# Performance work log

Measured on AMD Instinct MI355X. Metric: run time of the kernel, lower is better.

## Reference

```python
import jax, jax.numpy as jnp
import numpy as np

H = 1024
NH = 16
HD = H // NH
TEMP = 0.5
LN_EPS = 1e-5


def setup_inputs() -> dict:
    key = jax.random.key(0)
    ks = jax.random.split(key, 11)
    s = 1.0 / np.sqrt(H)
    return {
        "feat": jax.random.normal(ks[0], (4, 2048, H), dtype=jnp.float32),
        "qw": jax.random.uniform(ks[1], (H, H), jnp.float32, -s, s),
        "qb": jax.random.uniform(ks[2], (H,), jnp.float32, -s, s),
        "kw": jax.random.uniform(ks[3], (H, H), jnp.float32, -s, s),
        "kb": jax.random.uniform(ks[4], (H,), jnp.float32, -s, s),
        "vw": jax.random.uniform(ks[5], (H, H), jnp.float32, -s, s),
        "vb": jax.random.uniform(ks[6], (H,), jnp.float32, -s, s),
        "ow": jax.random.uniform(ks[7], (H, H), jnp.float32, -s, s),
        "ob": jax.random.uniform(ks[8], (H,), jnp.float32, -s, s),
        "ln_g": jnp.ones((H,), jnp.float32),
        "ln_b": jnp.zeros((H,), jnp.float32),
    }


def reference(feat, qw, qb, kw, kb, vw, vb, ow, ob, ln_g, ln_b):
    B, S, _ = feat.shape
    # torch Linear: y = x @ W.T + b
    def split_heads(x):  # [B,S,H] -> [B,NH,S,HD]
        return x.reshape(B, S, NH, HD).transpose(0, 2, 1, 3)

    Q = split_heads(feat @ qw.T + qb)
    K = split_heads(feat @ kw.T + kb)
    V = split_heads(feat @ vw.T + vb)

    # temperature-scaled attention (note: divide by 0.5, NOT 1/sqrt(d))
    scores = jnp.einsum("bhqd,bhkd->bhqk", Q, K) / TEMP
    w = jax.nn.softmax(scores, axis=-1)
    attn = jnp.einsum("bhqk,bhkd->bhqd", w, V)  # [B,NH,S,HD]
    attn = attn.transpose(0, 2, 1, 3).reshape(B, S, H)

    out = attn @ ow.T + ob
    out = jax.nn.relu(out)  # dropout is identity in eval mode
    mu = jnp.mean(out, axis=-1, keepdims=True)
    var = jnp.mean(jnp.square(out - mu), axis=-1, keepdims=True)
    out = (out - mu) * jax.lax.rsqrt(var + LN_EPS) * ln_g + ln_b
    return out
```

## Files before the change

### kernel.cpp

```cpp
#include <hip/hip_runtime.h>
#include <math.h>

#define HDIM 1024
#define NHEAD 16
#define HEADD 64
#define SEQLEN 2048
#define BATCH 4
#define MROWS (BATCH * SEQLEN)
#define LN_EPS 1e-5f
#define QSCALE 2.8853900817779268f

typedef float f32x4 __attribute__((ext_vector_type(4)));
typedef short s16x8 __attribute__((ext_vector_type(8)));
typedef short s16x4 __attribute__((ext_vector_type(4)));
typedef __bf16 bf16x4 __attribute__((ext_vector_type(4)));

#define MFMA16(a, b, c) __builtin_amdgcn_mfma_f32_16x16x32_bf16((a), (b), (c), 0, 0, 0)

#if __has_builtin(__builtin_amdgcn_exp2f)
#define EXP2(x) __builtin_amdgcn_exp2f(x)
#else
#define EXP2(x) exp2f(x)
#endif

__device__ __forceinline__ void load_lds16(const __bf16* g, __bf16* l) {
  __builtin_amdgcn_global_load_lds((const __attribute__((address_space(1))) void*)g,
                                   (__attribute__((address_space(3))) void*)l, 16, 0, 0);
}

__global__ __launch_bounds__(256) void split_k(const float* __restrict__ src,
                                               __bf16* __restrict__ h,
                                               __bf16* __restrict__ l, int n4) {
  int i = blockIdx.x * blockDim.x + threadIdx.x;
  if (i >= n4) return;
  float4 v = reinterpret_cast<const float4*>(src)[i];
  bf16x4 hv, lv;
  hv[0] = (__bf16)v.x; hv[1] = (__bf16)v.y; hv[2] = (__bf16)v.z; hv[3] = (__bf16)v.w;
  lv[0] = (__bf16)(v.x - (float)hv[0]);
  lv[1] = (__bf16)(v.y - (float)hv[1]);
  lv[2] = (__bf16)(v.z - (float)hv[2]);
  lv[3] = (__bf16)(v.w - (float)hv[3]);
  reinterpret_cast<bf16x4*>(h)[i] = hv;
  reinterpret_cast<bf16x4*>(l)[i] = lv;
}

__global__ __launch_bounds__(256) void wsplit_k(
    const float* __restrict__ w0, const float* __restrict__ w1,
    const float* __restrict__ w2, const float* __restrict__ w3,
    __bf16* __restrict__ h0, __bf16* __restrict__ l0, __bf16* __restrict__ h1,
    __bf16* __restrict__ l1, __bf16* __restrict__ h2, __bf16* __restrict__ l2,
    __bf16* __restrict__ h3, __bf16* __restrict__ l3) {
  const int which = blockIdx.y;
  const float* src = which == 0 ? w0 : which == 1 ? w1 : which == 2 ? w2 : w3;
  __bf16* h = which == 0 ? h0 : which == 1 ? h1 : which == 2 ? h2 : h3;
  __bf16* l = which == 0 ? l0 : which == 1 ? l1 : which == 2 ? l2 : l3;
  const int i = blockIdx.x * blockDim.x + threadIdx.x;
  float4 v = reinterpret_cast<const float4*>(src)[i];
  bf16x4 hv, lv;
  hv[0] = (__bf16)v.x; hv[1] = (__bf16)v.y; hv[2] = (__bf16)v.z; hv[3] = (__bf16)v.w;
  lv[0] = (__bf16)(v.x - (float)hv[0]);
  lv[1] = (__bf16)(v.y - (float)hv[1]);
  lv[2] = (__bf16)(v.z - (float)hv[2]);
  lv[3] = (__bf16)(v.w - (float)hv[3]);
  reinterpret_cast<bf16x4*>(h)[i] = hv;
  reinterpret_cast<bf16x4*>(l)[i] = lv;
}

template <int EPI, int PASSES>
__global__ __launch_bounds__(256, 2) void gemm3p_k(
    const __bf16* __restrict__ AH, const __bf16* __restrict__ AL,
    const __bf16* __restrict__ BH, const __bf16* __restrict__ BL,
    const float* __restrict__ bias, const float scale, __bf16* __restrict__ CH,
    __bf16* __restrict__ CL, float* __restrict__ CF) {
  __shared__ __bf16 smem[(PASSES == 3) ? 32768 : 24576];

  const int tid = threadIdx.x;
  const int lane = tid & 63;
  const int w = tid >> 6;
  const int fr = lane & 15;
  const int g = lane >> 4;
  const int wm = w >> 1, wn = w & 1;
  const int m0 = blockIdx.x << 7;
  const int n0 = blockIdx.y << 7;

#define GSTAGE(buf, kt)                                                       \
  do {                                                                        \
    const int ke_ = (kt) * 32 + (lane & 3) * 8;                               \
    _Pragma("unroll") for (int c_ = 0; c_ < 2; ++c_) {                        \
      const int rr_ = 32 * w + 16 * c_ + (lane >> 2);                         \
      const int lo_ = (32 * w + 16 * c_) * 32;                                \
      load_lds16(AH + (size_t)(m0 + rr_) * HDIM + ke_, &smem[(buf)*4096 + lo_]); \
      load_lds16(AL + (size_t)(m0 + rr_) * HDIM + ke_, &smem[8192 + (buf)*4096 + lo_]); \
      load_lds16(BH + (size_t)(n0 + rr_) * HDIM + ke_, &smem[16384 + (buf)*4096 + lo_]); \
      if (PASSES == 3)                                                        \
        load_lds16(BL + (size_t)(n0 + rr_) * HDIM + ke_, &smem[24576 + (buf)*4096 + lo_]); \
    }                                                                         \
  } while (0)

  f32x4 acc[4][4] = {};

  GSTAGE(0, 0);
  __syncthreads();

  for (int kt = 0; kt < HDIM / 32; ++kt) {
    const int buf = kt & 1;
    if (kt + 1 < HDIM / 32) GSTAGE(buf ^ 1, kt + 1);

    s16x8 aH[4], aL[4], bH[4], bL[4];
#pragma unroll
    for (int mi = 0; mi < 4; ++mi) {
      const int off = (wm * 64 + mi * 16 + fr) * 32 + g * 8;
      aH[mi] = *reinterpret_cast<const s16x8*>(&smem[buf * 4096 + off]);
      aL[mi] = *reinterpret_cast<const s16x8*>(&smem[8192 + buf * 4096 + off]);
    }
#pragma unroll
    for (int ni = 0; ni < 4; ++ni) {
      const int off = (wn * 64 + ni * 16 + fr) * 32 + g * 8;
      bH[ni] = *reinterpret_cast<const s16x8*>(&smem[16384 + buf * 4096 + off]);
      if (PASSES == 3)
        bL[ni] = *reinterpret_cast<const s16x8*>(&smem[24576 + buf * 4096 + off]);
    }
#pragma unroll
    for (int mi = 0; mi < 4; ++mi)
#pragma unroll
      for (int ni = 0; ni < 4; ++ni) {
        acc[mi][ni] = MFMA16(aH[mi], bH[ni], acc[mi][ni]);
        if (PASSES == 3) acc[mi][ni] = MFMA16(aH[mi], bL[ni], acc[mi][ni]);
        acc[mi][ni] = MFMA16(aL[mi], bH[ni], acc[mi][ni]);
      }
    __syncthreads();
  }

  float bv[4];
#pragma unroll
  for (int ni = 0; ni < 4; ++ni) bv[ni] = bias[n0 + wn * 64 + ni * 16 + fr];

  if (EPI == 0) {
#pragma unroll
    for (int mi = 0; mi < 4; ++mi)
#pragma unroll
      for (int ni = 0; ni < 4; ++ni)
#pragma unroll
        for (int r = 0; r < 4; ++r) {
          const float v = (acc[mi][ni][r] + bv[ni]) * scale;
          const int m = m0 + wm * 64 + mi * 16 + 4 * g + r;
          const int n = n0 + wn * 64 + ni * 16 + fr;
          const int b = m >> 11, s = m & 2047, h = n >> 6, d = n & 63;
          const size_t o = ((size_t)(b * NHEAD + h) * SEQLEN + s) * HEADD + d;
          const __bf16 hb = (__bf16)v;
          CH[o] = hb;
          CL[o] = (__bf16)(v - (float)hb);
        }
  } else if (EPI == 2) {
#pragma unroll
    for (int mi = 0; mi < 4; ++mi)
#pragma unroll
      for (int ni = 0; ni < 4; ++ni)
#pragma unroll
        for (int r = 0; r < 4; ++r) {
          const int m = m0 + wm * 64 + mi * 16 + 4 * g + r;
          const int n = n0 + wn * 64 + ni * 16 + fr;
          CF[(size_t)m * HDIM + n] = acc[mi][ni][r] + bv[ni];
        }
  } else {
    __syncthreads();
#pragma unroll
    for (int mi = 0; mi < 4; ++mi)
#pragma unroll
      for (int ni = 0; ni < 4; ++ni)
#pragma unroll
        for (int r = 0; r < 4; ++r) {
          const float v = acc[mi][ni][r] + bv[ni];
          const int nl = wn * 64 + ni * 16 + fr;
          const int ml = wm * 64 + mi * 16 + 4 * g + r;
          smem[nl * 128 + (((ml >> 3) ^ (nl & 7)) << 3) + (ml & 7)] = (__bf16)v;
        }
    __syncthreads();
    const int nl = tid >> 1, mh = tid & 1;
    const int b = m0 >> 11, s0 = m0 & 2047;
    const int gn = n0 + nl, h = gn >> 6, d = gn & 63;
#pragma unroll
    for (int j = 0; j < 8; ++j) {
      const int cm = mh * 8 + j;
      s16x8 vv = *reinterpret_cast<const s16x8*>(&smem[nl * 128 + ((cm ^ (nl & 7)) << 3)]);
      const size_t o = ((size_t)((b * NHEAD + h) * HEADD + d)) * SEQLEN + s0 + cm * 8;
      *reinterpret_cast<s16x8*>(&CH[o]) = vv;
    }
  }
#undef GSTAGE
}

__global__ __launch_bounds__(256, 3) void attn7_k(
    const __bf16* __restrict__ QH, const __bf16* __restrict__ QL,
    const __bf16* __restrict__ KH, const __bf16* __restrict__ KL,
    const __bf16* __restrict__ VT, __bf16* __restrict__ OH,
    __bf16* __restrict__ OL) {
  __shared__ __bf16 smem[24576];

  const int tid = threadIdx.x;
  const int lane = tid & 63;
  const int w = tid >> 6;
  const int fr = lane & 15;
  const int g = lane >> 4;
  const int f7 = fr & 7;

  const int blk = blockIdx.x;
  const int xcd = blk & 7, idx = blk >> 3;
  const int bh = xcd * 8 + (idx >> 4);
  const int qt = idx & 15;
  const int q0 = qt << 7;
  const size_t bhO = (size_t)bh * SEQLEN * HEADD;

  s16x8 qHf[2][2], qLf[2][2];
#pragma unroll
  for (int qb = 0; qb < 2; ++qb) {
    const size_t qoff = bhO + (size_t)(q0 + w * 32 + qb * 16 + fr) * HEADD;
#pragma unroll
    for (int ks = 0; ks < 2; ++ks) {
      qHf[qb][ks] = *reinterpret_cast<const s16x8*>(&QH[qoff + ks * 32 + g * 8]);
      qLf[qb][ks] = *reinterpret_cast<const s16x8*>(&QL[qoff + ks * 32 + g * 8]);
    }
  }

  const __bf16* gsrc[6];
  int gstep[6], ldoff[6];
  {
    const int rsub = lane >> 3;
    const int l7 = lane & 7;
#pragma unroll
    for (int i_ = 0; i_ < 6; ++i_) {
      const int L_ = w * 6 + i_;
      const int t_ = L_ >> 3, sub_ = L_ & 7;
      ldoff[i_] = t_ * 8192 + sub_ * 512;
      if (t_ < 2) {
        const __bf16* base_ = (t_ == 0) ? KH : KL;
        const int ch_ = l7 ^ (((sub_ & 3) << 1) | (rsub & 1));
        gsrc[i_] = base_ + bhO + (size_t)(sub_ * 8 + rsub) * HEADD + ch_ * 8;
        gstep[i_] = 64 * HEADD;
      } else {
        const int ch_ = l7 ^ rsub;
        gsrc[i_] = VT + ((size_t)bh * HEADD + sub_ * 8 + rsub) * SEQLEN + ch_ * 8;
        gstep[i_] = 64;
      }
    }
  }

#define ASTAGE(bufl)                                              \
  do {                                                            \
    _Pragma("unroll") for (int i_ = 0; i_ < 6; ++i_) {            \
      load_lds16(gsrc[i_], &smem[ldoff[i_] + (bufl)*4096]);       \
      gsrc[i_] += gstep[i_];                                      \
    }                                                             \
  } while (0)

  const int sK = ((fr >> 2) << 1) | (fr & 1);
  const int rbk0 = ((fr >> 2) * 8 + (fr & 3)) * 64 + ((g ^ sK) << 3);
  const int rbk1 = rbk0 ^ 32;
  const int rbv0 = fr * 64 + ((g ^ f7) << 3);
  const int rbv1 = rbv0 ^ 32;

  f32x4 oacc0[4] = {}, oacc1[4] = {};
  float m0r = -1e30f, m1r = -1e30f, l0r = 0.f, l1r = 0.f;

  auto process = [&](const int B) {
    f32x4 sf0[4] = {}, sf1[4] = {};
    __builtin_amdgcn_s_setprio(1);
#pragma unroll
    for (int kb = 0; kb < 4; ++kb) {
      const int ko = (kb & 1) * 256 + (kb >> 1) * 2048;
      const s16x8 kh0 = *reinterpret_cast<const s16x8*>(&smem[B * 4096 + ko + rbk0]);
      const s16x8 kl0 = *reinterpret_cast<const s16x8*>(&smem[8192 + B * 4096 + ko + rbk0]);
      const s16x8 kh1 = *reinterpret_cast<const s16x8*>(&smem[B * 4096 + ko + rbk1]);
      const s16x8 kl1 = *reinterpret_cast<const s16x8*>(&smem[8192 + B * 4096 + ko + rbk1]);
      sf0[kb] = MFMA16(kh0, qHf[0][0], sf0[kb]);
      sf0[kb] = MFMA16(kl0, qHf[0][0], sf0[kb]);
      sf0[kb] = MFMA16(kh0, qLf[0][0], sf0[kb]);
      sf0[kb] = MFMA16(kh1, qHf[0][1], sf0[kb]);
      sf0[kb] = MFMA16(kl1, qHf[0][1], sf0[kb]);
      sf0[kb] = MFMA16(kh1, qLf[0][1], sf0[kb]);
      sf1[kb] = MFMA16(kh0, qHf[1][0], sf1[kb]);
      sf1[kb] = MFMA16(kl0, qHf[1][0], sf1[kb]);
      sf1[kb] = MFMA16(kh0, qLf[1][0], sf1[kb]);
      sf1[kb] = MFMA16(kh1, qHf[1][1], sf1[kb]);
      sf1[kb] = MFMA16(kl1, qHf[1][1], sf1[kb]);
      sf1[kb] = MFMA16(kh1, qLf[1][1], sf1[kb]);
    }
    __builtin_amdgcn_s_setprio(0);

    float mx0 = sf0[0][0], mx1 = sf1[0][0];
#pragma unroll
    for (int kb = 0; kb < 4; ++kb)
#pragma unroll
      for (int r = 0; r < 4; ++r) {
        mx0 = fmaxf(mx0, sf0[kb][r]);
        mx1 = fmaxf(mx1, sf1[kb][r]);
      }
    mx0 = fmaxf(mx0, __shfl_xor(mx0, 16));
    mx0 = fmaxf(mx0, __shfl_xor(mx0, 32));
    mx1 = fmaxf(mx1, __shfl_xor(mx1, 16));
    mx1 = fmaxf(mx1, __shfl_xor(mx1, 32));
    const bool ok = (mx0 <= m0r + 11.5f) && (mx1 <= m1r + 11.5f);
    if (!__all(ok)) {
      const float mn0 = fmaxf(m0r, mx0), mn1 = fmaxf(m1r, mx1);
      const float c0 = EXP2(m0r - mn0), c1 = EXP2(m1r - mn1);
      m0r = mn0; m1r = mn1;
      l0r *= c0; l1r *= c1;
      float cr0[4], cr1[4];
#pragma unroll
      for (int r = 0; r < 4; ++r) {
        cr0[r] = __shfl(c0, 4 * g + r);
        cr1[r] = __shfl(c1, 4 * g + r);
      }
#pragma unroll
      for (int di = 0; di < 4; ++di)
#pragma unroll
        for (int r = 0; r < 4; ++r) {
          oacc0[di][r] *= cr0[r];
          oacc1[di][r] *= cr1[r];
        }
    }
    float ps0 = 0.f, ps1 = 0.f;
#pragma unroll
    for (int kb = 0; kb < 4; ++kb)
#pragma unroll
      for (int r = 0; r < 4; ++r) {
        const float p0 = EXP2(sf0[kb][r] - m0r);
        const float p1 = EXP2(sf1[kb][r] - m1r);
        sf0[kb][r] = p0;
        sf1[kb][r] = p1;
        ps0 += p0;
        ps1 += p1;
      }
    ps0 += __shfl_xor(ps0, 16);
    ps0 += __shfl_xor(ps0, 32);
    ps1 += __shfl_xor(ps1, 16);
    ps1 += __shfl_xor(ps1, 32);
    l0r += ps0;
    l1r += ps1;

    __builtin_amdgcn_s_setprio(1);
#pragma unroll
    for (int ks = 0; ks < 2; ++ks) {
      s16x8 pa0, pa1;
#pragma unroll
      for (int i = 0; i < 4; ++i) {
        pa0[i]     = __builtin_bit_cast(short, (__bf16)sf0[2 * ks][i]);
        pa0[i + 4] = __builtin_bit_cast(short, (__bf16)sf0[2 * ks + 1][i]);
        pa1[i]     = __builtin_bit_cast(short, (__bf16)sf1[2 * ks][i]);
        pa1[i + 4] = __builtin_bit_cast(short, (__bf16)sf1[2 * ks + 1][i]);
      }
      const int rbv = ks ? rbv1 : rbv0;
#pragma unroll
      for (int di = 0; di < 4; ++di) {
        const s16x8 vf = *reinterpret_cast<const s16x8*>(
            &smem[16384 + B * 4096 + di * 1024 + rbv]);
        oacc0[di] = MFMA16(pa0, vf, oacc0[di]);
        oacc1[di] = MFMA16(pa1, vf, oacc1[di]);
      }
    }
    __builtin_amdgcn_s_setprio(0);
  };

  ASTAGE(0);
  __syncthreads();
  for (int kt = 0; kt < SEQLEN / 64 - 2; kt += 2) {
    ASTAGE(1);
    process(0);
    __syncthreads();
    ASTAGE(0);
    process(1);
    __syncthreads();
  }
  ASTAGE(1);
  process(0);
  __syncthreads();
  process(1);

  const int b = bh >> 4, h = bh & 15;
  const float inv0 = 1.0f / l0r, inv1 = 1.0f / l1r;
  float iv0[4], iv1[4];
#pragma unroll
  for (int r = 0; r < 4; ++r) {
    iv0[r] = __shfl(inv0, 4 * g + r);
    iv1[r] = __shfl(inv1, 4 * g + r);
  }
#pragma unroll
  for (int di = 0; di < 4; ++di)
#pragma unroll
    for (int r = 0; r < 4; ++r) {
      const int srow = q0 + w * 32 + 4 * g + r;
      const size_t o0 = ((size_t)b * SEQLEN + srow) * HDIM + h * 64 + di * 16 + fr;
      const size_t o1 = o0 + 16 * HDIM;
      const float v0 = oacc0[di][r] * iv0[r];
      const float v1 = oacc1[di][r] * iv1[r];
      const __bf16 hb0 = (__bf16)v0;
      const __bf16 hb1 = (__bf16)v1;
      OH[o0] = hb0;
      OL[o0] = (__bf16)(v0 - (float)hb0);
      OH[o1] = hb1;
      OL[o1] = (__bf16)(v1 - (float)hb1);
    }
#undef ASTAGE
}

__global__ __launch_bounds__(256) void relu_ln_k(const float* __restrict__ X,
                                                 const float* __restrict__ gam,
                                                 const float* __restrict__ bta,
                                                 float* __restrict__ out) {
  __shared__ float red[8];
  const int row = blockIdx.x;
  const int tid = threadIdx.x;
  const int c = tid << 2;

  const float4 v = *reinterpret_cast<const float4*>(&X[(size_t)row * HDIM + c]);
  float x[4] = {fmaxf(v.x, 0.f), fmaxf(v.y, 0.f), fmaxf(v.z, 0.f), fmaxf(v.w, 0.f)};
  float sum = x[0] + x[1] + x[2] + x[3];
  float ss = x[0] * x[0] + x[1] * x[1] + x[2] * x[2] + x[3] * x[3];
#pragma unroll
  for (int off = 1; off < 64; off <<= 1) {
    sum += __shfl_xor(sum, off);
    ss += __shfl_xor(ss, off);
  }
  const int wid = tid >> 6;
  if ((tid & 63) == 0) {
    red[wid] = sum;
    red[4 + wid] = ss;
  }
  __syncthreads();
  sum = red[0] + red[1] + red[2] + red[3];
  ss = red[4] + red[5] + red[6] + red[7];
  const float mean = sum * (1.0f / HDIM);
  const float var = ss * (1.0f / HDIM) - mean * mean;
  const float rstd = rsqrtf(var + LN_EPS);

  const float4 gv = *reinterpret_cast<const float4*>(&gam[c]);
  const float4 bv = *reinterpret_cast<const float4*>(&bta[c]);
  float4 o;
  o.x = (x[0] - mean) * rstd * gv.x + bv.x;
  o.y = (x[1] - mean) * rstd * gv.y + bv.y;
  o.z = (x[2] - mean) * rstd * gv.z + bv.z;
  o.w = (x[3] - mean) * rstd * gv.w + bv.w;
  *reinterpret_cast<float4*>(&out[(size_t)row * HDIM + c]) = o;
}

extern "C" void kernel_launch(void* const* d_in, const int* in_sizes, int n_in,
                              void* d_out, int out_size, void* d_ws, size_t ws_size,
                              hipStream_t stream) {
  const float* feat = (const float*)d_in[0];
  const float* qw = (const float*)d_in[1];
  const float* qb = (const float*)d_in[2];
  const float* kw = (const float*)d_in[3];
  const float* kb = (const float*)d_in[4];
  const float* vw = (const float*)d_in[5];
  const float* vb = (const float*)d_in[6];
  const float* ow = (const float*)d_in[7];
  const float* ob = (const float*)d_in[8];
  const float* ln_g = (const float*)d_in[9];
  const float* ln_b = (const float*)d_in[10];

  char* ws = (char*)d_ws;
  const size_t MB = 1u << 20;
  __bf16* qwH = (__bf16*)(ws + 0 * MB);
  __bf16* kwH = (__bf16*)(ws + 2 * MB);
  __bf16* vwH = (__bf16*)(ws + 4 * MB);
  __bf16* owH = (__bf16*)(ws + 6 * MB);
  __bf16* qwL = (__bf16*)(ws + 8 * MB);
  __bf16* kwL = (__bf16*)(ws + 10 * MB);
  __bf16* vwL = (__bf16*)(ws + 12 * MB);
  __bf16* owL = (__bf16*)(ws + 14 * MB);
  __bf16* QHp = (__bf16*)(ws + 16 * MB);
  __bf16* QLp = (__bf16*)(ws + 32 * MB);
  __bf16* KHp = (__bf16*)(ws + 48 * MB);
  __bf16* KLp = (__bf16*)(ws + 64 * MB);
  __bf16* VTp = (__bf16*)(ws + 80 * MB);
  __bf16* ftH = (__bf16*)(ws + 96 * MB);
  __bf16* ftL = (__bf16*)(ws + 112 * MB);
  __bf16* atH = ftH;
  __bf16* atL = ftL;
  float* proj = (float*)(ws + 16 * MB);

  split_k<<<(MROWS * HDIM / 4 + 255) / 256, 256, 0, stream>>>(feat, ftH, ftL,
                                                              MROWS * HDIM / 4);
  wsplit_k<<<dim3(HDIM * HDIM / 4 / 256, 4), 256, 0, stream>>>(
      qw, kw, vw, ow, qwH, qwL, kwH, kwL, vwH, vwL, owH, owL);

  const dim3 gg(MROWS / 128, HDIM / 128);
  gemm3p_k<0, 3><<<gg, 256, 0, stream>>>(ftH, ftL, qwH, qwL, qb, QSCALE, QHp, QLp, nullptr);
  gemm3p_k<0, 3><<<gg, 256, 0, stream>>>(ftH, ftL, kwH, kwL, kb, 1.0f, KHp, KLp, nullptr);
  gemm3p_k<1, 2><<<gg, 256, 0, stream>>>(ftH, ftL, vwH, vwL, vb, 1.0f, VTp, nullptr, nullptr);

  attn7_k<<<BATCH * NHEAD * (SEQLEN / 128), 256, 0, stream>>>(QHp, QLp, KHp, KLp,
                                                              VTp, atH, atL);

  gemm3p_k<2, 2><<<gg, 256, 0, stream>>>(atH, atL, owH, owL, ob, 1.0f, nullptr,
                                         nullptr, proj);

  relu_ln_k<<<MROWS, 256, 0, stream>>>(proj, ln_g, ln_b, (float*)d_out);
}
```

Before: 443.9 us.

## Use fp16 for V and P in attention, stage output via LDS, re-swizzle K

The V-transpose epilogue now stores V as fp16 instead of bf16, and the P·V MFMAs switch to the f16 variant with P converted to fp16, which gives more mantissa bits at the same MFMA cost. The attention output is first staged through LDS as packed hi/lo pairs and then written with 16-byte vector stores instead of scattered 2-byte stores. The K LDS swizzle pattern also changes, aimed at reducing bank conflicts. The fp16 path adds a risk of overflow in V, which is small for these inputs.

```diff
diff --git a/kernel.cpp b/kernel.cpp
--- a/kernel.cpp
+++ b/kernel.cpp
@@ -14,8 +14,10 @@
 typedef short s16x8 __attribute__((ext_vector_type(8)));
 typedef short s16x4 __attribute__((ext_vector_type(4)));
 typedef __bf16 bf16x4 __attribute__((ext_vector_type(4)));
+typedef _Float16 f16x8 __attribute__((ext_vector_type(8)));
 
 #define MFMA16(a, b, c) __builtin_amdgcn_mfma_f32_16x16x32_bf16((a), (b), (c), 0, 0, 0)
+#define MFMA16H(a, b, c) __builtin_amdgcn_mfma_f32_16x16x32_f16((a), (b), (c), 0, 0, 0)
 
 #if __has_builtin(__builtin_amdgcn_exp2f)
 #define EXP2(x) __builtin_amdgcn_exp2f(x)
@@ -164,6 +166,7 @@
         }
   } else {
     __syncthreads();
+    short* sm = reinterpret_cast<short*>(smem);
 #pragma unroll
     for (int mi = 0; mi < 4; ++mi)
 #pragma unroll
@@ -173,7 +176,8 @@
           const float v = acc[mi][ni][r] + bv[ni];
           const int nl = wn * 64 + ni * 16 + fr;
           const int ml = wm * 64 + mi * 16 + 4 * g + r;
-          smem[nl * 128 + (((ml >> 3) ^ (nl & 7)) << 3) + (ml & 7)] = (__bf16)v;
+          sm[nl * 128 + (((ml >> 3) ^ (nl & 7)) << 3) + (ml & 7)] =
+              __builtin_bit_cast(short, (_Float16)v);
         }
     __syncthreads();
     const int nl = tid >> 1, mh = tid & 1;
@@ -182,7 +186,7 @@
 #pragma unroll
     for (int j = 0; j < 8; ++j) {
       const int cm = mh * 8 + j;
-      s16x8 vv = *reinterpret_cast<const s16x8*>(&smem[nl * 128 + ((cm ^ (nl & 7)) << 3)]);
+      s16x8 vv = *reinterpret_cast<const s16x8*>(&sm[nl * 128 + ((cm ^ (nl & 7)) << 3)]);
       const size_t o = ((size_t)((b * NHEAD + h) * HEADD + d)) * SEQLEN + s0 + cm * 8;
       *reinterpret_cast<s16x8*>(&CH[o]) = vv;
     }
@@ -190,7 +194,7 @@
 #undef GSTAGE
 }
 
-__global__ __launch_bounds__(256, 3) void attn7_k(
+__global__ __launch_bounds__(256, 3) void attn8_k(
     const __bf16* __restrict__ QH, const __bf16* __restrict__ QL,
     const __bf16* __restrict__ KH, const __bf16* __restrict__ KL,
     const __bf16* __restrict__ VT, __bf16* __restrict__ OH,
@@ -234,7 +238,7 @@
       ldoff[i_] = t_ * 8192 + sub_ * 512;
       if (t_ < 2) {
         const __bf16* base_ = (t_ == 0) ? KH : KL;
-        const int ch_ = l7 ^ (((sub_ & 3) << 1) | (rsub & 1));
+        const int ch_ = l7 ^ (((sub_ & 1) << 2) | (rsub & 3));
         gsrc[i_] = base_ + bhO + (size_t)(sub_ * 8 + rsub) * HEADD + ch_ * 8;
         gstep[i_] = 64 * HEADD;
       } else {
@@ -253,7 +257,7 @@
     }                                                             \
   } while (0)
 
-  const int sK = ((fr >> 2) << 1) | (fr & 1);
+  const int sK = (((fr >> 2) & 1) << 2) | (fr & 3);
   const int rbk0 = ((fr >> 2) * 8 + (fr & 3)) * 64 + ((g ^ sK) << 3);
   const int rbk1 = rbk0 ^ 32;
   const int rbv0 = fr * 64 + ((g ^ f7) << 3);
@@ -341,21 +345,22 @@
     __builtin_amdgcn_s_setprio(1);
 #pragma unroll
     for (int ks = 0; ks < 2; ++ks) {
-      s16x8 pa0, pa1;
+      f16x8 pa0, pa1;
 #pragma unroll
       for (int i = 0; i < 4; ++i) {
-        pa0[i]     = __builtin_bit_cast(short, (__bf16)sf0[2 * ks][i]);
-        pa0[i + 4] = __builtin_bit_cast(short, (__bf16)sf0[2 * ks + 1][i]);
-        pa1[i]     = __builtin_bit_cast(short, (__bf16)sf1[2 * ks][i]);
-        pa1[i + 4] = __builtin_bit_cast(short, (__bf16)sf1[2 * ks + 1][i]);
+        pa0[i]     = (_Float16)sf0[2 * ks][i];
+        pa0[i + 4] = (_Float16)sf0[2 * ks + 1][i];
+        pa1[i]     = (_Float16)sf1[2 * ks][i];
+        pa1[i + 4] = (_Float16)sf1[2 * ks + 1][i];
       }
       const int rbv = ks ? rbv1 : rbv0;
 #pragma unroll
       for (int di = 0; di < 4; ++di) {
-        const s16x8 vf = *reinterpret_cast<const s16x8*>(
+        const s16x8 vraw = *reinterpret_cast<const s16x8*>(
             &smem[16384 + B * 4096 + di * 1024 + rbv]);
-        oacc0[di] = MFMA16(pa0, vf, oacc0[di]);
-        oacc1[di] = MFMA16(pa1, vf, oacc1[di]);
+        const f16x8 vf = __builtin_bit_cast(f16x8, vraw);
+        oacc0[di] = MFMA16H(pa0, vf, oacc0[di]);
+        oacc1[di] = MFMA16H(pa1, vf, oacc1[di]);
       }
     }
     __builtin_amdgcn_s_setprio(0);
@@ -384,22 +389,55 @@
     iv0[r] = __shfl(inv0, 4 * g + r);
     iv1[r] = __shfl(inv1, 4 * g + r);
   }
+  __syncthreads();
+  uint32_t* Lb = reinterpret_cast<uint32_t*>(smem);
 #pragma unroll
   for (int di = 0; di < 4; ++di)
 #pragma unroll
     for (int r = 0; r < 4; ++r) {
-      const int srow = q0 + w * 32 + 4 * g + r;
-      const size_t o0 = ((size_t)b * SEQLEN + srow) * HDIM + h * 64 + di * 16 + fr;
-      const size_t o1 = o0 + 16 * HDIM;
-      const float v0 = oacc0[di][r] * iv0[r];
-      const float v1 = oacc1[di][r] * iv1[r];
-      const __bf16 hb0 = (__bf16)v0;
-      const __bf16 hb1 = (__bf16)v1;
-      OH[o0] = hb0;
-      OL[o0] = (__bf16)(v0 - (float)hb0);
-      OH[o1] = hb1;
-      OL[o1] = (__bf16)(v1 - (float)hb1);
-    }
+      const int c = di * 16 + fr;
+      {
+        const float v = oacc0[di][r] * iv0[r];
+        const __bf16 hb = (__bf16)v;
+        const __bf16 lb = (__bf16)(v - (float)hb);
+        const int lr = w * 32 + 4 * g + r;
+        Lb[lr * 68 + c] = (uint32_t)(unsigned short)__builtin_bit_cast(short, hb) |
+                          ((uint32_t)(unsigned short)__builtin_bit_cast(short, lb) << 16);
+      }
+      {
+        const float v = oacc1[di][r] * iv1[r];
+        const __bf16 hb = (__bf16)v;
+        const __bf16 lb = (__bf16)(v - (float)hb);
+        const int lr = w * 32 + 16 + 4 * g + r;
+        Lb[lr * 68 + c] = (uint32_t)(unsigned short)__builtin_bit_cast(short, hb) |
+                          ((uint32_t)(unsigned short)__builtin_bit_cast(short, lb) << 16);
+      }
+    }
+  __syncthreads();
+  {
+    const int lr = tid >> 1;
+    const int c0 = (tid & 1) * 32;
+    const size_t obase = ((size_t)b * SEQLEN + q0 + lr) * HDIM + h * 64 + c0;
+    uint32_t x[32];
+#pragma unroll
+    for (int k = 0; k < 8; ++k)
+      *reinterpret_cast<uint4*>(&x[4 * k]) =
+          *reinterpret_cast<const uint4*>(&Lb[lr * 68 + c0 + 4 * k]);
+#pragma unroll
+    for (int k = 0; k < 4; ++k) {
+      uint4 hq, lq;
+      hq.x = (x[8 * k + 0] & 0xffffu) | (x[8 * k + 1] << 16);
+      hq.y = (x[8 * k + 2] & 0xffffu) | (x[8 * k + 3] << 16);
+      hq.z = (x[8 * k + 4] & 0xffffu) | (x[8 * k + 5] << 16);
+      hq.w = (x[8 * k + 6] & 0xffffu) | (x[8 * k + 7] << 16);
+      lq.x = (x[8 * k + 0] >> 16) | (x[8 * k + 1] & 0xffff0000u);
+      lq.y = (x[8 * k + 2] >> 16) | (x[8 * k + 3] & 0xffff0000u);
+      lq.z = (x[8 * k + 4] >> 16) | (x[8 * k + 5] & 0xffff0000u);
+      lq.w = (x[8 * k + 6] >> 16) | (x[8 * k + 7] & 0xffff0000u);
+      *reinterpret_cast<uint4*>(&OH[obase + 8 * k]) = hq;
+      *reinterpret_cast<uint4*>(&OL[obase + 8 * k]) = lq;
+    }
+  }
 #undef ASTAGE
 }
 
@@ -489,7 +527,7 @@
   gemm3p_k<0, 3><<<gg, 256, 0, stream>>>(ftH, ftL, kwH, kwL, kb, 1.0f, KHp, KLp, nullptr);
   gemm3p_k<1, 2><<<gg, 256, 0, stream>>>(ftH, ftL, vwH, vwL, vb, 1.0f, VTp, nullptr, nullptr);
 
-  attn7_k<<<BATCH * NHEAD * (SEQLEN / 128), 256, 0, stream>>>(QHp, QLp, KHp, KLp,
+  attn8_k<<<BATCH * NHEAD * (SEQLEN / 128), 256, 0, stream>>>(QHp, QLp, KHp, KLp,
                                                               VTp, atH, atL);
 
   gemm3p_k<2, 2><<<gg, 256, 0, stream>>>(atH, atL, owH, owL, ob, 1.0f, nullptr,
```

Result: no change. 450.3 us (+1.4%).
